# Optimization experiments

Hardware: AMD Instinct MI355X
Metric: run time of the kernel (lower is better)

Reference implementation:

```python
import jax, jax.numpy as jnp
from jax import lax
import numpy as np

T, I, H = 8192, 256, 1024  # timesteps, input_dim, hidden_dim


def setup_inputs() -> dict:
    key = jax.random.key(0)
    ks = jax.random.split(key, 7)
    s = 1.0 / np.sqrt(H)  # PyTorch LSTM init scale
    return {
        "sequence": jax.random.normal(ks[0], (T, I), jnp.float32),
        "W_ih": jax.random.uniform(ks[1], (4 * H, I), jnp.float32, -s, s),
        "W_hh": jax.random.uniform(ks[2], (4 * H, H), jnp.float32, -s, s),
        "b_ih": jax.random.uniform(ks[3], (4 * H,), jnp.float32, -s, s),
        "b_hh": jax.random.uniform(ks[4], (4 * H,), jnp.float32, -s, s),
        "W_out": jax.random.uniform(ks[5], (1, H), jnp.float32, -s, s),
        "b_out": jax.random.uniform(ks[6], (1,), jnp.float32, -s, s),
    }


def reference(sequence, W_ih, W_hh, b_ih, b_hh, W_out, b_out):
    hdim = W_hh.shape[1]
    # Precompute input projection for all timesteps in one GEMM: [T, 4H]
    x_gates = sequence @ W_ih.T + (b_ih + b_hh)

    def step(carry, xg):
        h, c = carry
        g = xg + h @ W_hh.T  # [4H], gate order i,f,g,o (PyTorch)
        i, f, gg, o = jnp.split(g, 4)
        i = jax.nn.sigmoid(i)
        f = jax.nn.sigmoid(f)
        gg = jnp.tanh(gg)
        o = jax.nn.sigmoid(o)
        c = f * c + i * gg
        h = o * jnp.tanh(c)
        return (h, c), h

    h0 = jnp.zeros((hdim,), sequence.dtype)
    c0 = jnp.zeros((hdim,), sequence.dtype)
    _, hs = lax.scan(step, (h0, c0), x_gates)  # hs: [T, H]
    out = hs @ W_out.T + b_out  # [T, 1]
    return jax.nn.sigmoid(out)
```

## Files before the change

kernel.cpp:

```cpp
#include <hip/hip_runtime.h>
#include <cstdint>
#include <cstddef>


#define T_STEPS 8192
#define IDIM 256
#define HDIM 1024
#define NWG 64
#define TPB 256

typedef _Float16 h2_t __attribute__((ext_vector_type(2)));

#if defined(__has_builtin)
#if __has_builtin(__builtin_amdgcn_fdot2)
#define HAS_FDOT2 1
#endif
#endif

__device__ __forceinline__ float fdot2(uint32_t a, uint32_t b, float c) {
#ifdef HAS_FDOT2
  return __builtin_amdgcn_fdot2(__builtin_bit_cast(h2_t, a),
                                __builtin_bit_cast(h2_t, b), c, false);
#else
  const h2_t av = __builtin_bit_cast(h2_t, a);
  const h2_t bv = __builtin_bit_cast(h2_t, b);
  c = fmaf((float)av[0], (float)bv[0], c);
  c = fmaf((float)av[1], (float)bv[1], c);
  return c;
#endif
}
__device__ __forceinline__ uint32_t packf16(float a, float b) {
  h2_t v;
  v[0] = (_Float16)a;
  v[1] = (_Float16)b;
  return __builtin_bit_cast(uint32_t, v);
}
__device__ __forceinline__ float sigmoidf_(float x) {
  return 1.0f / (1.0f + __expf(-x));
}
__device__ __forceinline__ float tanhf_(float x) {
  return 1.0f - 2.0f / (1.0f + __expf(2.0f * x));
}

__global__ __launch_bounds__(TPB, 1) void lstm_persistent(
    const float* __restrict__ seq, const float* __restrict__ Wih,
    const float* __restrict__ Whh, const float* __restrict__ bih,
    const float* __restrict__ bhh, const float* __restrict__ Wout,
    const float* __restrict__ bout, float* __restrict__ out,
    uint32_t* __restrict__ ring) {
  const int wg = blockIdx.x;
  const int tid = threadIdx.x;
  const int w = tid >> 6;
  const int l = tid & 63;

  __shared__ uint32_t zbuf[640];
  __shared__ float red[4][64];
  __shared__ uint32_t wlds[512];

  {
    float4 wv = *(const float4*)(Wout + tid * 4);
    wlds[tid * 2] = packf16(wv.x, wv.y);
    wlds[tid * 2 + 1] = packf16(wv.z, wv.w);
  }
  const float b_out0 = bout[0];

  const int grow = (l >> 4) * HDIM + wg * 16 + (l & 15);
  const float bias_l = bih[grow] + bhh[grow];
  const float* whrow = Whh + (size_t)grow * HDIM;
  const float* wirow = Wih + (size_t)grow * IDIM;
  const int cbase = w * 320;
  uint32_t wreg[160];
#pragma unroll
  for (int j = 0; j < 160; ++j) {
    const int c = cbase + 2 * j;
    float a, b;
    if (c < HDIM) {
      a = whrow[c];
      b = whrow[c + 1];
    } else {
      a = wirow[c - HDIM];
      b = wirow[c - HDIM + 1];
    }
    wreg[j] = packf16(a, b);
  }

  float c_st = 0.0f;

  for (int t = 0; t <= T_STEPS; ++t) {
    __syncthreads();

    if (t < T_STEPS && tid >= 64 && tid < 128) {
      const int q = tid - 64;
      float4 xv = *(const float4*)(seq + (size_t)t * IDIM + q * 4);
      zbuf[512 + q * 2] = packf16(xv.x, xv.y);
      zbuf[512 + q * 2 + 1] = packf16(xv.z, xv.w);
    }

    if (t > 0) {
      const int ps = (t - 1) & 1;
      const uint32_t tg = (uint32_t)((t - 1) & 3);
      const uint64_t want = (uint64_t)tg * 0x0000000100000001ull;
      const uint64_t msk = 0x0000000300000003ull;
      const uint64_t* hp = (const uint64_t*)(ring + ps * HDIM + tid * 4);
      uint64_t v0, v1;
      int guard = 0;
      for (;;) {
        v0 = __hip_atomic_load(hp + 0, __ATOMIC_RELAXED, __HIP_MEMORY_SCOPE_AGENT);
        v1 = __hip_atomic_load(hp + 1, __ATOMIC_RELAXED, __HIP_MEMORY_SCOPE_AGENT);
        if (((v0 & msk) == want) && ((v1 & msk) == want)) break;
        if (++guard > (1 << 22)) break;
      }
      const float a0 = __uint_as_float((uint32_t)v0);
      const float a1 = __uint_as_float((uint32_t)(v0 >> 32));
      const float a2 = __uint_as_float((uint32_t)v1);
      const float a3 = __uint_as_float((uint32_t)(v1 >> 32));
      zbuf[tid * 2] = packf16(a0, a1);
      zbuf[tid * 2 + 1] = packf16(a2, a3);
    } else {
      zbuf[tid * 2] = 0u;
      zbuf[tid * 2 + 1] = 0u;
    }
    __syncthreads();

    if (t < T_STEPS) {
      float ac0 = 0.f, ac1 = 0.f, ac2 = 0.f, ac3 = 0.f;
      const uint32_t* zb = zbuf + w * 160;
#pragma unroll
      for (int jj = 0; jj < 40; ++jj) {
        const uint4 zv = *(const uint4*)(zb + jj * 4);
        ac0 = fdot2(wreg[jj * 4 + 0], zv.x, ac0);
        ac1 = fdot2(wreg[jj * 4 + 1], zv.y, ac1);
        ac2 = fdot2(wreg[jj * 4 + 2], zv.z, ac2);
        ac3 = fdot2(wreg[jj * 4 + 3], zv.w, ac3);
      }
      red[w][l] = (ac0 + ac1) + (ac2 + ac3);
      __syncthreads();

      if (w == 0) {
        const float g = red[0][l] + red[1][l] + red[2][l] + red[3][l] + bias_l;
        const int uu = l & 15;
        const float gi = __shfl(g, uu);
        const float gf = __shfl(g, uu + 16);
        const float gg = __shfl(g, uu + 32);
        const float go = __shfl(g, uu + 48);
        if (l < 16) {
          const float is = sigmoidf_(gi);
          const float fs = sigmoidf_(gf);
          const float gt = tanhf_(gg);
          const float os = sigmoidf_(go);
          c_st = fs * c_st + is * gt;
          const float hv = os * tanhf_(c_st);
          const uint32_t hb = (__float_as_uint(hv) & ~3u) | (uint32_t)(t & 3);
          __hip_atomic_store(ring + (t & 1) * HDIM + wg * 16 + l, hb,
                             __ATOMIC_RELAXED, __HIP_MEMORY_SCOPE_AGENT);
        }
      }
    }

    if (t > 0 && w == 1 && ((t - 1) & (NWG - 1)) == wg) {
      float o0 = 0.f, o1 = 0.f;
#pragma unroll
      for (int j = 0; j < 8; j += 2) {
        o0 = fdot2(wlds[l * 8 + j], zbuf[l * 8 + j], o0);
        o1 = fdot2(wlds[l * 8 + j + 1], zbuf[l * 8 + j + 1], o1);
      }
      float o = o0 + o1;
#pragma unroll
      for (int off = 32; off >= 1; off >>= 1) o += __shfl_xor(o, off);
      if (l == 0) out[t - 1] = sigmoidf_(o + b_out0);
    }
  }
}

extern "C" void kernel_launch(void* const* d_in, const int* in_sizes, int n_in,
                              void* d_out, int out_size, void* d_ws, size_t ws_size,
                              hipStream_t stream) {
  const float* seq = (const float*)d_in[0];
  const float* Wih = (const float*)d_in[1];
  const float* Whh = (const float*)d_in[2];
  const float* bih = (const float*)d_in[3];
  const float* bhh = (const float*)d_in[4];
  const float* Wout = (const float*)d_in[5];
  const float* bout = (const float*)d_in[6];

  uint32_t* ring = (uint32_t*)d_ws;

  hipMemsetAsync(d_ws, 0xAA, 2 * HDIM * sizeof(uint32_t), stream);

  lstm_persistent<<<NWG, TPB, 0, stream>>>(seq, Wih, Whh, bih, bhh, Wout, bout,
                                           (float*)d_out, ring);
}
```

Measured before the change: 16.16 ms.

## Make each wavefront independent to remove per-step workgroup barriers

Work is repartitioned so each wavefront owns 4 hidden units. Within a wavefront, the four lanes per gate row split the reduction dimension and combine their partial sums with shuffles instead of a shared-memory reduction across wavefronts. Every wavefront polls the global ring itself and keeps a private LDS copy of h and x, so all __syncthreads inside the time loop are gone. The intent is to cut barrier latency on the serial critical path. The cost is four times as much polling traffic on the ring, duplicated packing work, and a wave-local ordering that relies on an explicit lgkmcnt wait.

```diff
diff --git a/kernel.cpp b/kernel.cpp
--- a/kernel.cpp
+++ b/kernel.cpp
@@ -52,10 +52,10 @@
   const int tid = threadIdx.x;
   const int w = tid >> 6;
   const int l = tid & 63;
-
-  __shared__ uint32_t zbuf[640];
-  __shared__ float red[4][64];
-  __shared__ uint32_t wlds[512];
+  const int gwid = (wg << 2) | w;
+
+  __shared__ alignas(16) uint32_t zbuf[4][640];
+  __shared__ alignas(16) uint32_t wlds[512];
 
   {
     float4 wv = *(const float4*)(Wout + tid * 4);
@@ -64,15 +64,17 @@
   }
   const float b_out0 = bout[0];
 
-  const int grow = (l >> 4) * HDIM + wg * 16 + (l & 15);
+  const int rl = l >> 2;
+  const int q = l & 3;
+  const int grow = (rl >> 2) * HDIM + wg * 16 + w * 4 + (rl & 3);
   const float bias_l = bih[grow] + bhh[grow];
   const float* whrow = Whh + (size_t)grow * HDIM;
   const float* wirow = Wih + (size_t)grow * IDIM;
-  const int cbase = w * 320;
+  const int cbase = q * 320;
   uint32_t wreg[160];
 #pragma unroll
-  for (int j = 0; j < 160; ++j) {
-    const int c = cbase + 2 * j;
+  for (int j2 = 0; j2 < 160; ++j2) {
+    const int c = cbase + 2 * j2;
     float a, b;
     if (c < HDIM) {
       a = whrow[c];
@@ -81,90 +83,105 @@
       a = wirow[c - HDIM];
       b = wirow[c - HDIM + 1];
     }
-    wreg[j] = packf16(a, b);
+    wreg[j2] = packf16(a, b);
   }
 
+  __syncthreads();
+
+  uint32_t* const zb = zbuf[w];
   float c_st = 0.0f;
+  int dead = 0;
 
   for (int t = 0; t <= T_STEPS; ++t) {
-    __syncthreads();
-
-    if (t < T_STEPS && tid >= 64 && tid < 128) {
-      const int q = tid - 64;
-      float4 xv = *(const float4*)(seq + (size_t)t * IDIM + q * 4);
-      zbuf[512 + q * 2] = packf16(xv.x, xv.y);
-      zbuf[512 + q * 2 + 1] = packf16(xv.z, xv.w);
-    }
+    float4 xv = make_float4(0.f, 0.f, 0.f, 0.f);
+    if (t < T_STEPS) xv = *(const float4*)(seq + (size_t)t * IDIM + 4 * l);
 
     if (t > 0) {
-      const int ps = (t - 1) & 1;
-      const uint32_t tg = (uint32_t)((t - 1) & 3);
-      const uint64_t want = (uint64_t)tg * 0x0000000100000001ull;
+      const uint64_t want = (uint64_t)((t - 1) & 3) * 0x0000000100000001ull;
       const uint64_t msk = 0x0000000300000003ull;
-      const uint64_t* hp = (const uint64_t*)(ring + ps * HDIM + tid * 4);
-      uint64_t v0, v1;
-      int guard = 0;
-      for (;;) {
-        v0 = __hip_atomic_load(hp + 0, __ATOMIC_RELAXED, __HIP_MEMORY_SCOPE_AGENT);
-        v1 = __hip_atomic_load(hp + 1, __ATOMIC_RELAXED, __HIP_MEMORY_SCOPE_AGENT);
-        if (((v0 & msk) == want) && ((v1 & msk) == want)) break;
-        if (++guard > (1 << 22)) break;
+      const uint64_t* hp =
+          (const uint64_t*)(ring + ((t - 1) & 1) * HDIM + 16 * l);
+      uint64_t v[8] = {0, 0, 0, 0, 0, 0, 0, 0};
+      if (!dead) {
+        int guard = 0;
+        for (;;) {
+#pragma unroll
+          for (int k = 0; k < 8; ++k)
+            v[k] = __hip_atomic_load(hp + k, __ATOMIC_RELAXED,
+                                     __HIP_MEMORY_SCOPE_AGENT);
+          bool ok = true;
+#pragma unroll
+          for (int k = 0; k < 8; ++k) ok = ok && ((v[k] & msk) == want);
+          if (ok) break;
+          if (++guard > (1 << 20)) { dead = 1; break; }
+        }
       }
-      const float a0 = __uint_as_float((uint32_t)v0);
-      const float a1 = __uint_as_float((uint32_t)(v0 >> 32));
-      const float a2 = __uint_as_float((uint32_t)v1);
-      const float a3 = __uint_as_float((uint32_t)(v1 >> 32));
-      zbuf[tid * 2] = packf16(a0, a1);
-      zbuf[tid * 2 + 1] = packf16(a2, a3);
+      uint32_t pk[8];
+#pragma unroll
+      for (int k = 0; k < 8; ++k)
+        pk[k] = packf16(__uint_as_float((uint32_t)v[k]),
+                        __uint_as_float((uint32_t)(v[k] >> 32)));
+      *(uint4*)(zb + 8 * l) = *(const uint4*)(pk);
+      *(uint4*)(zb + 8 * l + 4) = *(const uint4*)(pk + 4);
     } else {
-      zbuf[tid * 2] = 0u;
-      zbuf[tid * 2 + 1] = 0u;
-    }
-    __syncthreads();
+      const uint4 z4 = {0u, 0u, 0u, 0u};
+      *(uint4*)(zb + 8 * l) = z4;
+      *(uint4*)(zb + 8 * l + 4) = z4;
+    }
+    if (t < T_STEPS) {
+      zb[512 + 2 * l] = packf16(xv.x, xv.y);
+      zb[512 + 2 * l + 1] = packf16(xv.z, xv.w);
+    }
+    asm volatile("s_waitcnt lgkmcnt(0)" ::: "memory");
+    __builtin_amdgcn_sched_barrier(0);
 
     if (t < T_STEPS) {
       float ac0 = 0.f, ac1 = 0.f, ac2 = 0.f, ac3 = 0.f;
-      const uint32_t* zb = zbuf + w * 160;
-#pragma unroll
-      for (int jj = 0; jj < 40; ++jj) {
-        const uint4 zv = *(const uint4*)(zb + jj * 4);
-        ac0 = fdot2(wreg[jj * 4 + 0], zv.x, ac0);
-        ac1 = fdot2(wreg[jj * 4 + 1], zv.y, ac1);
-        ac2 = fdot2(wreg[jj * 4 + 2], zv.z, ac2);
-        ac3 = fdot2(wreg[jj * 4 + 3], zv.w, ac3);
+      const uint32_t* zs = zb + 160 * q;
+#pragma unroll
+      for (int k = 0; k < 40; ++k) {
+        const uint4 zv = *(const uint4*)(zs + 4 * k);
+        ac0 = fdot2(wreg[4 * k + 0], zv.x, ac0);
+        ac1 = fdot2(wreg[4 * k + 1], zv.y, ac1);
+        ac2 = fdot2(wreg[4 * k + 2], zv.z, ac2);
+        ac3 = fdot2(wreg[4 * k + 3], zv.w, ac3);
       }
-      red[w][l] = (ac0 + ac1) + (ac2 + ac3);
-      __syncthreads();
-
-      if (w == 0) {
-        const float g = red[0][l] + red[1][l] + red[2][l] + red[3][l] + bias_l;
-        const int uu = l & 15;
-        const float gi = __shfl(g, uu);
-        const float gf = __shfl(g, uu + 16);
-        const float gg = __shfl(g, uu + 32);
-        const float go = __shfl(g, uu + 48);
-        if (l < 16) {
-          const float is = sigmoidf_(gi);
-          const float fs = sigmoidf_(gf);
-          const float gt = tanhf_(gg);
-          const float os = sigmoidf_(go);
-          c_st = fs * c_st + is * gt;
-          const float hv = os * tanhf_(c_st);
-          const uint32_t hb = (__float_as_uint(hv) & ~3u) | (uint32_t)(t & 3);
-          __hip_atomic_store(ring + (t & 1) * HDIM + wg * 16 + l, hb,
-                             __ATOMIC_RELAXED, __HIP_MEMORY_SCOPE_AGENT);
-        }
+      float s = (ac0 + ac1) + (ac2 + ac3);
+      s += __shfl_xor(s, 1);
+      s += __shfl_xor(s, 2);
+      const float g = s + bias_l;
+      const int j = l & 3;
+      const float gi = __shfl(g, 4 * j);
+      const float gf = __shfl(g, 16 + 4 * j);
+      const float gg = __shfl(g, 32 + 4 * j);
+      const float go = __shfl(g, 48 + 4 * j);
+      const float is = sigmoidf_(gi);
+      const float fs = sigmoidf_(gf);
+      const float gt = tanhf_(gg);
+      const float os = sigmoidf_(go);
+      c_st = fs * c_st + is * gt;
+      const float hv = os * tanhf_(c_st);
+      if (l < 4) {
+        const uint32_t hb = (__float_as_uint(hv) & ~3u) | (uint32_t)(t & 3);
+        __hip_atomic_store(ring + (t & 1) * HDIM + wg * 16 + w * 4 + l, hb,
+                           __ATOMIC_RELAXED, __HIP_MEMORY_SCOPE_AGENT);
       }
     }
 
-    if (t > 0 && w == 1 && ((t - 1) & (NWG - 1)) == wg) {
-      float o0 = 0.f, o1 = 0.f;
-#pragma unroll
-      for (int j = 0; j < 8; j += 2) {
-        o0 = fdot2(wlds[l * 8 + j], zbuf[l * 8 + j], o0);
-        o1 = fdot2(wlds[l * 8 + j + 1], zbuf[l * 8 + j + 1], o1);
-      }
-      float o = o0 + o1;
+    if (t > 0 && gwid == ((t - 1) & 255)) {
+      const uint4 wv0 = *(const uint4*)(wlds + 8 * l);
+      const uint4 wv1 = *(const uint4*)(wlds + 8 * l + 4);
+      const uint4 zv0 = *(const uint4*)(zb + 8 * l);
+      const uint4 zv1 = *(const uint4*)(zb + 8 * l + 4);
+      float o = 0.f;
+      o = fdot2(wv0.x, zv0.x, o);
+      o = fdot2(wv0.y, zv0.y, o);
+      o = fdot2(wv0.z, zv0.z, o);
+      o = fdot2(wv0.w, zv0.w, o);
+      o = fdot2(wv1.x, zv1.x, o);
+      o = fdot2(wv1.y, zv1.y, o);
+      o = fdot2(wv1.z, zv1.z, o);
+      o = fdot2(wv1.w, zv1.w, o);
 #pragma unroll
       for (int off = 32; off >= 1; off >>= 1) o += __shfl_xor(o, off);
       if (l == 0) out[t - 1] = sigmoidf_(o + b_out0);
```

After: 19.35 ms. 1.2x slower.
